# Performance work log

Measured on AMD Instinct MI355X. Metric: run time of the kernel, lower is better.

## Reference

```python
import jax, jax.numpy as jnp
import numpy as np

QDIM = 32
H = 512
B = 65536
BIAS = 2.0
N_TRIL = QDIM * (QDIM + 1) // 2  # 528 total params per sample
TRIL_R, TRIL_C = np.tril_indices(QDIM, -1)  # strictly-lower entries (500)
DIAG = np.arange(QDIM)


def setup_inputs() -> dict:
    key = jax.random.key(0)
    ks = jax.random.split(key, 12)
    def lin(k, fan_in, fan_out):
        return jax.random.normal(k, (fan_in, fan_out), dtype=jnp.float32) / np.sqrt(fan_in).astype(np.float32)
    return {
        "q": jax.random.normal(ks[0], (B, QDIM), dtype=jnp.float32),
        # ResMLP embed: input linear, two residual hidden blocks, output linear
        "W_in": lin(ks[1], QDIM, H), "b_in": jnp.zeros((H,), jnp.float32),
        "W_h1": lin(ks[2], H, H),    "b_h1": jnp.zeros((H,), jnp.float32),
        "W_h2": lin(ks[3], H, H),    "b_h2": jnp.zeros((H,), jnp.float32),
        "W_out": lin(ks[4], H, H),   "b_out": jnp.zeros((H,), jnp.float32),
        # Cholesky parameter head: H -> qdim*(qdim+1)/2
        "W_o": lin(ks[5], H, N_TRIL), "b_o": jnp.zeros((N_TRIL,), jnp.float32),
    }


def reference(q, W_in, b_in, W_h1, b_h1, W_h2, b_h2, W_out, b_out, W_o, b_o):
    # ResMLP embed (relu, residual connections on equal-width hidden layers)
    x = jax.nn.relu(q @ W_in + b_in)               # [B, H]
    x = jax.nn.relu(x @ W_h1 + b_h1) + x           # residual block 1
    x = jax.nn.relu(x @ W_h2 + b_h2) + x           # residual block 2
    embed = x @ W_out + b_out                      # [B, H]
    # Cholesky factor params
    L_params = embed @ W_o + b_o                   # [B, 528]
    L_diag = L_params[:, :QDIM] + BIAS             # [B, 32]
    L_tril = L_params[:, QDIM:]                    # [B, 496+... strictly lower]
    Bsz = q.shape[0]
    L = jnp.zeros((Bsz, QDIM, QDIM), L_params.dtype)
    L = L.at[:, TRIL_R, TRIL_C].set(L_tril)        # bfill_lowertriangle
    L = L.at[:, DIAG, DIAG].set(L_diag)            # bfill_diagonal
    M = L @ jnp.swapaxes(L, -1, -2)                # SPD mass matrix [B, 32, 32]
    return M
```

## Files before the change

### kernel.cpp

```cpp
#include <hip/hip_runtime.h>
#include <math.h>

typedef __bf16 bf16;
typedef bf16 bf16x2 __attribute__((ext_vector_type(2)));
typedef bf16 bf16x4 __attribute__((ext_vector_type(4)));
typedef bf16 bf16x8 __attribute__((ext_vector_type(8)));
typedef float f32x4 __attribute__((ext_vector_type(4)));

#define BATCH 65536
#define QD 32
#define HD 512
#define NT 528
#define BM 64
#define BIAS_C 2.0f

#define OFF_WIN  0
#define OFF_WH1  16384
#define OFF_WH2  278528
#define OFF_WOUT 540672
#define OFF_WO   802816
#define WT_TOTAL 1073152
#define N_TILES  2096

#define MFMA(a, b, c) __builtin_amdgcn_mfma_f32_16x16x32_bf16((a), (b), (c), 0, 0, 0)

__global__ __launch_bounds__(256) void prep_weights(
    const float* __restrict__ W_in, const float* __restrict__ W_h1,
    const float* __restrict__ W_h2, const float* __restrict__ W_out,
    const float* __restrict__ W_o, bf16* __restrict__ wt)
{
    const int bt = blockIdx.x;

    __shared__ float lds[32][17];
    const float* src; int ld, nt, kt;
    if (bt < 32)        { src = W_in;                 nt = bt;     kt = 0;      ld = HD; }
    else if (bt < 544)  { int t = bt - 32;   src = W_h1;  nt = t >> 4; kt = t & 15; ld = HD; }
    else if (bt < 1056) { int t = bt - 544;  src = W_h2;  nt = t >> 4; kt = t & 15; ld = HD; }
    else if (bt < 1568) { int t = bt - 1056; src = W_out; nt = t >> 4; kt = t & 15; ld = HD; }
    else                { int t = bt - 1568; src = W_o;   nt = t >> 4; kt = t & 15; ld = NT; }

    const int s = threadIdx.x * 2;
    {
        int ki = s >> 4, fi = s & 15;
        const float* p = src + (size_t)(kt * 32 + ki) * ld + nt * 16 + fi;
        lds[ki][fi]     = p[0];
        lds[ki][fi + 1] = p[1];
    }
    __syncthreads();
    {
        int fi = s >> 5, ki = s & 31;
        bf16x2 w;
        w[0] = (bf16)lds[ki][fi];
        w[1] = (bf16)lds[ki + 1][fi];
        *(bf16x2*)(wt + (size_t)bt * 512 + s) = w;
    }
}

__device__ __forceinline__ int xbyte(int m, int f) {
    return m * 1024 + ((((f >> 3)) ^ m) << 4) + ((f & 7) << 1);
}

__device__ __forceinline__ int lbyte(int il, int r, int c) {
    return il * 2048 + r * 64 + ((((c >> 3)) ^ (r & 3) ^ (il & 3)) << 4) + ((c & 7) << 1);
}

__device__ __forceinline__ void p2rc(int p, int& r_, int& c_) {
    if (p < QD) { r_ = p; c_ = p; }
    else {
        int t = p - QD;
        r_ = (int)((1.0f + sqrtf(8.0f * (float)t + 1.0f)) * 0.5f);
        while (r_ * (r_ - 1) / 2 > t) --r_;
        while ((r_ + 1) * r_ / 2 <= t) ++r_;
        c_ = t - r_ * (r_ - 1) / 2;
    }
}

__global__ __launch_bounds__(512, 4) void fused_kernel(
    const float* __restrict__ q,
    const float* __restrict__ b_in, const float* __restrict__ b_h1,
    const float* __restrict__ b_h2, const float* __restrict__ b_out,
    const float* __restrict__ b_o,
    const bf16* __restrict__ wt, float* __restrict__ out)
{
    __shared__ __attribute__((aligned(16))) unsigned char smem[65536];
    const int tid  = threadIdx.x;
    const int lane = tid & 63;
    const int wave = tid >> 6;
    const int l15  = lane & 15;
    const int quad = lane >> 4;
    const int blk  = blockIdx.x;

    const f32x4 zf = {0.f, 0.f, 0.f, 0.f};
    f32x4 acc[4][4];

    {
        bf16x8 bfr[4];
        #pragma unroll
        for (int ct = 0; ct < 4; ++ct) {
            const float* qp = q + (size_t)(blk * 64 + ct * 16 + l15) * QD + quad * 8;
            f32x4 lo = *(const f32x4*)qp;
            f32x4 hi = *(const f32x4*)(qp + 4);
            bf16x8 b;
            #pragma unroll
            for (int j = 0; j < 4; ++j) { b[j] = (bf16)lo[j]; b[4 + j] = (bf16)hi[j]; }
            bfr[ct] = b;
        }
        #pragma unroll
        for (int rt = 0; rt < 4; ++rt) {
            bf16x8 a = *(const bf16x8*)(wt + OFF_WIN + (wave * 4 + rt) * 512 + l15 * 32 + quad * 8);
            #pragma unroll
            for (int ct = 0; ct < 4; ++ct)
                acc[rt][ct] = MFMA(a, bfr[ct], zf);
        }
        #pragma unroll
        for (int rt = 0; rt < 4; ++rt) {
            int f0 = wave * 64 + rt * 16 + quad * 4;
            f32x4 bias = *(const f32x4*)(b_in + f0);
            #pragma unroll
            for (int ct = 0; ct < 4; ++ct) {
                int m = ct * 16 + l15;
                bf16x4 w;
                #pragma unroll
                for (int r = 0; r < 4; ++r) {
                    float v = acc[rt][ct][r] + bias[r];
                    v = v > 0.f ? v : 0.f;
                    w[r] = (bf16)v;
                }
                *(bf16x4*)(smem + xbyte(m, f0)) = w;
            }
        }
    }
    __syncthreads();

    const bf16*  WL[3] = { wt + OFF_WH1, wt + OFF_WH2, wt + OFF_WOUT };
    const float* BL[3] = { b_h1, b_h2, b_out };
    #pragma unroll
    for (int L = 0; L < 3; ++L) {
        #pragma unroll
        for (int rt = 0; rt < 4; ++rt)
            #pragma unroll
            for (int ct = 0; ct < 4; ++ct)
                acc[rt][ct] = zf;
        const bf16* W = WL[L];
        #pragma unroll 2
        for (int kk = 0; kk < 16; ++kk) {
            bf16x8 bfr2[4];
            #pragma unroll
            for (int ct = 0; ct < 4; ++ct) {
                int m = ct * 16 + l15;
                bfr2[ct] = *(const bf16x8*)(smem + m * 1024 + (((kk * 4 + quad) ^ m) << 4));
            }
            #pragma unroll
            for (int rt = 0; rt < 4; ++rt) {
                bf16x8 a = *(const bf16x8*)(W + ((wave * 4 + rt) * 16 + kk) * 512 + l15 * 32 + quad * 8);
                #pragma unroll
                for (int ct = 0; ct < 4; ++ct)
                    acc[rt][ct] = MFMA(a, bfr2[ct], acc[rt][ct]);
            }
        }
        __syncthreads();
        {
            const float* Bv = BL[L];
            #pragma unroll
            for (int rt = 0; rt < 4; ++rt) {
                int f0 = wave * 64 + rt * 16 + quad * 4;
                f32x4 bias = *(const f32x4*)(Bv + f0);
                #pragma unroll
                for (int ct = 0; ct < 4; ++ct) {
                    int m = ct * 16 + l15;
                    unsigned char* p = smem + xbyte(m, f0);
                    bf16x4 w;
                    if (L < 2) {
                        bf16x4 old = *(const bf16x4*)p;
                        #pragma unroll
                        for (int r = 0; r < 4; ++r) {
                            float v = acc[rt][ct][r] + bias[r];
                            v = v > 0.f ? v : 0.f;
                            v += (float)old[r];
                            w[r] = (bf16)v;
                        }
                    } else {
                        #pragma unroll
                        for (int r = 0; r < 4; ++r) {
                            float v = acc[rt][ct][r] + bias[r];
                            w[r] = (bf16)v;
                        }
                    }
                    *(bf16x4*)p = w;
                }
            }
        }
        __syncthreads();
    }

    f32x4 acc_ex = zf;
    #pragma unroll
    for (int rt = 0; rt < 4; ++rt)
        #pragma unroll
        for (int ct = 0; ct < 4; ++ct)
            acc[rt][ct] = zf;
    #pragma unroll 2
    for (int kk = 0; kk < 16; ++kk) {
        bf16x8 bfr2[4];
        #pragma unroll
        for (int ct = 0; ct < 4; ++ct) {
            int m = ct * 16 + l15;
            bfr2[ct] = *(const bf16x8*)(smem + m * 1024 + (((kk * 4 + quad) ^ m) << 4));
        }
        #pragma unroll
        for (int rt = 0; rt < 4; ++rt) {
            bf16x8 a = *(const bf16x8*)(wt + OFF_WO + ((wave * 4 + rt) * 16 + kk) * 512 + l15 * 32 + quad * 8);
            #pragma unroll
            for (int ct = 0; ct < 4; ++ct)
                acc[rt][ct] = MFMA(a, bfr2[ct], acc[rt][ct]);
        }
        if (wave >= 4) {
            bf16x8 aex = *(const bf16x8*)(wt + OFF_WO + (32 * 16 + kk) * 512 + l15 * 32 + quad * 8);
            if (wave == 4) acc_ex = MFMA(aex, bfr2[0], acc_ex);
            else if (wave == 5) acc_ex = MFMA(aex, bfr2[1], acc_ex);
            else if (wave == 6) acc_ex = MFMA(aex, bfr2[2], acc_ex);
            else acc_ex = MFMA(aex, bfr2[3], acc_ex);
        }
    }
    __syncthreads();

    #pragma unroll
    for (int rt = 0; rt < 4; ++rt) {
        f32x4 b = *(const f32x4*)(b_o + wave * 64 + rt * 16 + quad * 4);
        if (rt < 2 && wave == 0) {
            #pragma unroll
            for (int r = 0; r < 4; ++r) b[r] += BIAS_C;
        }
        #pragma unroll
        for (int ct = 0; ct < 4; ++ct)
            #pragma unroll
            for (int r = 0; r < 4; ++r)
                acc[rt][ct][r] += b[r];
    }
    if (wave >= 4) {
        f32x4 be = *(const f32x4*)(b_o + 512 + quad * 4);
        #pragma unroll
        for (int r = 0; r < 4; ++r) acc_ex[r] += be[r];
    }

    int loff[4][4];
    #pragma unroll
    for (int rt = 0; rt < 4; ++rt)
        #pragma unroll
        for (int r = 0; r < 4; ++r) {
            int rr, cc;
            p2rc(wave * 64 + rt * 16 + quad * 4 + r, rr, cc);
            loff[rt][r] = lbyte(l15, rr, cc);
        }
    int loffex[4] = {0, 0, 0, 0};
    if (wave >= 4) {
        #pragma unroll
        for (int r = 0; r < 4; ++r) {
            int rr, cc;
            p2rc(512 + quad * 4 + r, rr, cc);
            loffex[r] = lbyte(l15, rr, cc);
        }
    }

    {
        unsigned long long* z = (unsigned long long*)smem;
        #pragma unroll
        for (int i = 0; i < 16; ++i) z[tid + 512 * i] = 0ull;
    }
    __syncthreads();

    #pragma unroll
    for (int g = 0; g < 4; ++g) {
        #pragma unroll
        for (int rt = 0; rt < 4; ++rt) {
            #pragma unroll
            for (int r = 0; r < 4; ++r) {
                float v = acc[rt][g][r];
                bf16 hi = (bf16)v;
                bf16 lo = (bf16)(v - (float)hi);
                int off = loff[rt][r];
                *(bf16*)(smem + off) = hi;
                *(bf16*)(smem + 32768 + off) = lo;
            }
        }
        if (wave == 4 + g) {
            #pragma unroll
            for (int r = 0; r < 4; ++r) {
                float v = acc_ex[r];
                bf16 hi = (bf16)v;
                bf16 lo = (bf16)(v - (float)hi);
                int off = loffex[r];
                *(bf16*)(smem + off) = hi;
                *(bf16*)(smem + 32768 + off) = lo;
            }
        }
        __syncthreads();
        #pragma unroll
        for (int ii = 0; ii < 2; ++ii) {
            const int it = wave + ii * 8;
            bf16x8 Fh[2], Fl[2];
            #pragma unroll
            for (int tl = 0; tl < 2; ++tl) {
                int m = tl * 16 + l15;
                int ch = quad ^ (m & 3) ^ (it & 3);
                int off = it * 2048 + m * 64 + (ch << 4);
                Fh[tl] = *(const bf16x8*)(smem + off);
                Fl[tl] = *(const bf16x8*)(smem + 32768 + off);
            }
            long base = ((long)(blk * 64 + g * 16 + it)) * 1024;
            #pragma unroll
            for (int mt = 0; mt < 2; ++mt) {
                #pragma unroll
                for (int nt = 0; nt < 2; ++nt) {
                    f32x4 mm = MFMA(Fh[mt], Fh[nt], zf);
                    mm = MFMA(Fh[mt], Fl[nt], mm);
                    mm = MFMA(Fl[mt], Fh[nt], mm);
                    #pragma unroll
                    for (int r = 0; r < 4; ++r)
                        out[base + (long)(mt * 16 + quad * 4 + r) * 32 + nt * 16 + l15] = mm[r];
                }
            }
        }
        __syncthreads();
    }
}

extern "C" void kernel_launch(void* const* d_in, const int* in_sizes, int n_in,
                              void* d_out, int out_size, void* d_ws, size_t ws_size,
                              hipStream_t stream)
{
    const float* q     = (const float*)d_in[0];
    const float* W_in  = (const float*)d_in[1];
    const float* b_in  = (const float*)d_in[2];
    const float* W_h1  = (const float*)d_in[3];
    const float* b_h1  = (const float*)d_in[4];
    const float* W_h2  = (const float*)d_in[5];
    const float* b_h2  = (const float*)d_in[6];
    const float* W_out = (const float*)d_in[7];
    const float* b_out = (const float*)d_in[8];
    const float* W_o   = (const float*)d_in[9];
    const float* b_o   = (const float*)d_in[10];
    float* out = (float*)d_out;
    bf16* wt = (bf16*)d_ws;

    prep_weights<<<N_TILES, 256, 0, stream>>>(W_in, W_h1, W_h2, W_out, W_o, wt);
    fused_kernel<<<BATCH / BM, 512, 0, stream>>>(q, b_in, b_h1, b_h2, b_out, b_o, wt, out);
}
```

Baseline: 470.1 us.

## Double-buffer weight fragment loads in GEMM loops and reswizzle Cholesky LDS layout

Software-pipelines the global weight fragment loads in the hidden-layer and output-head GEMM loops. The next k-step's A fragments are prefetched into a second register set while MFMAs on the current set run, to hide global/L2 load latency. It also changes the LDS XOR swizzle for the Cholesky factor tiles to cut bank conflicts, and hoists all Fh/Fl LDS reads ahead of the M=LL^T MFMAs. These changes raise register pressure under the 512-thread, 4-block launch bounds, which could cause spills or lower occupancy.

```diff
diff --git a/kernel.cpp b/kernel.cpp
--- a/kernel.cpp
+++ b/kernel.cpp
@@ -61,7 +61,9 @@
 }
 
 __device__ __forceinline__ int lbyte(int il, int r, int c) {
-    return il * 2048 + r * 64 + ((((c >> 3)) ^ (r & 3) ^ (il & 3)) << 4) + ((c & 7) << 1);
+    int ch = (c >> 3) ^ (r & 3) ^ ((r >> 2) & 3) ^ (il & 3);
+    int by = (c & 7) ^ ((il >> 2) << 1);
+    return il * 2048 + r * 64 + (ch << 4) + (by << 1);
 }
 
 __device__ __forceinline__ void p2rc(int p, int& r_, int& c_) {
@@ -141,9 +143,16 @@
             #pragma unroll
             for (int ct = 0; ct < 4; ++ct)
                 acc[rt][ct] = zf;
-        const bf16* W = WL[L];
+        const bf16* wbase = WL[L] + (size_t)(wave * 4) * 16 * 512 + l15 * 32 + quad * 8;
+        bf16x8 aA[4], aB[4];
+        #pragma unroll
+        for (int rt = 0; rt < 4; ++rt)
+            aA[rt] = *(const bf16x8*)(wbase + (rt * 16 + 0) * 512);
         #pragma unroll 2
-        for (int kk = 0; kk < 16; ++kk) {
+        for (int kk = 0; kk < 16; kk += 2) {
+            #pragma unroll
+            for (int rt = 0; rt < 4; ++rt)
+                aB[rt] = *(const bf16x8*)(wbase + (rt * 16 + kk + 1) * 512);
             bf16x8 bfr2[4];
             #pragma unroll
             for (int ct = 0; ct < 4; ++ct) {
@@ -151,12 +160,25 @@
                 bfr2[ct] = *(const bf16x8*)(smem + m * 1024 + (((kk * 4 + quad) ^ m) << 4));
             }
             #pragma unroll
-            for (int rt = 0; rt < 4; ++rt) {
-                bf16x8 a = *(const bf16x8*)(W + ((wave * 4 + rt) * 16 + kk) * 512 + l15 * 32 + quad * 8);
+            for (int rt = 0; rt < 4; ++rt)
                 #pragma unroll
                 for (int ct = 0; ct < 4; ++ct)
-                    acc[rt][ct] = MFMA(a, bfr2[ct], acc[rt][ct]);
-            }
+                    acc[rt][ct] = MFMA(aA[rt], bfr2[ct], acc[rt][ct]);
+            if (kk < 14) {
+                #pragma unroll
+                for (int rt = 0; rt < 4; ++rt)
+                    aA[rt] = *(const bf16x8*)(wbase + (rt * 16 + kk + 2) * 512);
+            }
+            #pragma unroll
+            for (int ct = 0; ct < 4; ++ct) {
+                int m = ct * 16 + l15;
+                bfr2[ct] = *(const bf16x8*)(smem + m * 1024 + ((((kk + 1) * 4 + quad) ^ m) << 4));
+            }
+            #pragma unroll
+            for (int rt = 0; rt < 4; ++rt)
+                #pragma unroll
+                for (int ct = 0; ct < 4; ++ct)
+                    acc[rt][ct] = MFMA(aB[rt], bfr2[ct], acc[rt][ct]);
         }
         __syncthreads();
         {
@@ -199,27 +221,58 @@
         #pragma unroll
         for (int ct = 0; ct < 4; ++ct)
             acc[rt][ct] = zf;
-    #pragma unroll 2
-    for (int kk = 0; kk < 16; ++kk) {
-        bf16x8 bfr2[4];
-        #pragma unroll
-        for (int ct = 0; ct < 4; ++ct) {
-            int m = ct * 16 + l15;
-            bfr2[ct] = *(const bf16x8*)(smem + m * 1024 + (((kk * 4 + quad) ^ m) << 4));
-        }
-        #pragma unroll
-        for (int rt = 0; rt < 4; ++rt) {
-            bf16x8 a = *(const bf16x8*)(wt + OFF_WO + ((wave * 4 + rt) * 16 + kk) * 512 + l15 * 32 + quad * 8);
-            #pragma unroll
-            for (int ct = 0; ct < 4; ++ct)
-                acc[rt][ct] = MFMA(a, bfr2[ct], acc[rt][ct]);
-        }
-        if (wave >= 4) {
-            bf16x8 aex = *(const bf16x8*)(wt + OFF_WO + (32 * 16 + kk) * 512 + l15 * 32 + quad * 8);
-            if (wave == 4) acc_ex = MFMA(aex, bfr2[0], acc_ex);
-            else if (wave == 5) acc_ex = MFMA(aex, bfr2[1], acc_ex);
-            else if (wave == 6) acc_ex = MFMA(aex, bfr2[2], acc_ex);
-            else acc_ex = MFMA(aex, bfr2[3], acc_ex);
+    {
+        const bf16* wbase = wt + OFF_WO + (size_t)(wave * 4) * 16 * 512 + l15 * 32 + quad * 8;
+        const bf16* exbase = wt + OFF_WO + (size_t)(32 * 16) * 512 + l15 * 32 + quad * 8;
+        bf16x8 aA[4], aB[4];
+        #pragma unroll
+        for (int rt = 0; rt < 4; ++rt)
+            aA[rt] = *(const bf16x8*)(wbase + (rt * 16 + 0) * 512);
+        #pragma unroll 2
+        for (int kk = 0; kk < 16; kk += 2) {
+            #pragma unroll
+            for (int rt = 0; rt < 4; ++rt)
+                aB[rt] = *(const bf16x8*)(wbase + (rt * 16 + kk + 1) * 512);
+            bf16x8 bfr2[4];
+            #pragma unroll
+            for (int ct = 0; ct < 4; ++ct) {
+                int m = ct * 16 + l15;
+                bfr2[ct] = *(const bf16x8*)(smem + m * 1024 + (((kk * 4 + quad) ^ m) << 4));
+            }
+            #pragma unroll
+            for (int rt = 0; rt < 4; ++rt)
+                #pragma unroll
+                for (int ct = 0; ct < 4; ++ct)
+                    acc[rt][ct] = MFMA(aA[rt], bfr2[ct], acc[rt][ct]);
+            if (wave >= 4) {
+                bf16x8 aex = *(const bf16x8*)(exbase + kk * 512);
+                if (wave == 4) acc_ex = MFMA(aex, bfr2[0], acc_ex);
+                else if (wave == 5) acc_ex = MFMA(aex, bfr2[1], acc_ex);
+                else if (wave == 6) acc_ex = MFMA(aex, bfr2[2], acc_ex);
+                else acc_ex = MFMA(aex, bfr2[3], acc_ex);
+            }
+            if (kk < 14) {
+                #pragma unroll
+                for (int rt = 0; rt < 4; ++rt)
+                    aA[rt] = *(const bf16x8*)(wbase + (rt * 16 + kk + 2) * 512);
+            }
+            #pragma unroll
+            for (int ct = 0; ct < 4; ++ct) {
+                int m = ct * 16 + l15;
+                bfr2[ct] = *(const bf16x8*)(smem + m * 1024 + ((((kk + 1) * 4 + quad) ^ m) << 4));
+            }
+            #pragma unroll
+            for (int rt = 0; rt < 4; ++rt)
+                #pragma unroll
+                for (int ct = 0; ct < 4; ++ct)
+                    acc[rt][ct] = MFMA(aB[rt], bfr2[ct], acc[rt][ct]);
+            if (wave >= 4) {
+                bf16x8 aex = *(const bf16x8*)(exbase + (kk + 1) * 512);
+                if (wave == 4) acc_ex = MFMA(aex, bfr2[0], acc_ex);
+                else if (wave == 5) acc_ex = MFMA(aex, bfr2[1], acc_ex);
+                else if (wave == 6) acc_ex = MFMA(aex, bfr2[2], acc_ex);
+                else acc_ex = MFMA(aex, bfr2[3], acc_ex);
+            }
         }
     }
     __syncthreads();
@@ -295,26 +348,30 @@
             }
         }
         __syncthreads();
+        bf16x8 Fh[2][2], Fl[2][2];
         #pragma unroll
         for (int ii = 0; ii < 2; ++ii) {
             const int it = wave + ii * 8;
-            bf16x8 Fh[2], Fl[2];
             #pragma unroll
             for (int tl = 0; tl < 2; ++tl) {
                 int m = tl * 16 + l15;
-                int ch = quad ^ (m & 3) ^ (it & 3);
+                int ch = quad ^ (m & 3) ^ ((m >> 2) & 3) ^ (it & 3);
                 int off = it * 2048 + m * 64 + (ch << 4);
-                Fh[tl] = *(const bf16x8*)(smem + off);
-                Fl[tl] = *(const bf16x8*)(smem + 32768 + off);
-            }
+                Fh[ii][tl] = *(const bf16x8*)(smem + off);
+                Fl[ii][tl] = *(const bf16x8*)(smem + 32768 + off);
+            }
+        }
+        #pragma unroll
+        for (int ii = 0; ii < 2; ++ii) {
+            const int it = wave + ii * 8;
             long base = ((long)(blk * 64 + g * 16 + it)) * 1024;
             #pragma unroll
             for (int mt = 0; mt < 2; ++mt) {
                 #pragma unroll
                 for (int nt = 0; nt < 2; ++nt) {
-                    f32x4 mm = MFMA(Fh[mt], Fh[nt], zf);
-                    mm = MFMA(Fh[mt], Fl[nt], mm);
-                    mm = MFMA(Fl[mt], Fh[nt], mm);
+                    f32x4 mm = MFMA(Fh[ii][mt], Fh[ii][nt], zf);
+                    mm = MFMA(Fh[ii][mt], Fl[ii][nt], mm);
+                    mm = MFMA(Fl[ii][mt], Fh[ii][nt], mm);
                     #pragma unroll
                     for (int r = 0; r < 4; ++r)
                         out[base + (long)(mt * 16 + quad * 4 + r) * 32 + nt * 16 + l15] = mm[r];
```

Result: slower. 679.8 us (+44.6%).
